# Optimization experiments

Hardware: AMD Instinct MI355X
Metric: run time of the kernel (lower is better)

The kernel has to match this reference:

```python
import jax, jax.numpy as jnp
import numpy as np

N, E, DIN, DH, DE, DOUT, G = 100000, 1600000, 64, 128, 16, 1, 256

def setup_inputs() -> dict:
    key = jax.random.key(0)
    ks = jax.random.split(key, 16)
    p = lambda k, s: (jax.random.normal(k, s, dtype=jnp.float32) * 0.05)
    return {
        "x": jax.random.normal(ks[0], (N, DIN), dtype=jnp.float32),
        "edge_index": jax.random.randint(ks[1], (2, E), 0, N, dtype=jnp.int64),
        "edge_attr": jax.random.normal(ks[2], (E, DE), dtype=jnp.float32),
        "batch": jnp.sort(jax.random.randint(ks[3], (N,), 0, G, dtype=jnp.int64)),
        # GINEConv 1: edge lin (edge_dim -> input_dim) + mlp1 (DIN->DH->DH)
        "ew1": p(ks[4], (DIN, DE)), "eb1": p(ks[5], (DIN,)),
        "w1a": p(ks[6], (DH, DIN)), "b1a": p(ks[7], (DH,)),
        "w1b": p(ks[8], (DH, DH)), "b1b": p(ks[9], (DH,)),
        # GINEConv 2: edge lin (edge_dim -> hidden_dim) + mlp2 (DH->DH->DH)
        "ew2": p(ks[10], (DH, DE)), "eb2": p(ks[11], (DH,)),
        "w2a": p(ks[12], (DH, DH)), "b2a": p(ks[13], (DH,)),
        "w2b": p(ks[14], (DH, DH)), "b2b": p(ks[15], (DH,)),
        "wf": p(jax.random.fold_in(key, 99), (DOUT, DH)),
        "bf": jnp.zeros((DOUT,), dtype=jnp.float32),
    }

def _gine(x, src, dst, edge_attr, ew, eb, wa, ba, wb, bb):
    # message = relu(x[src] + Lin(edge_attr)); sum-aggregate at dst; eps=0
    msg = jax.nn.relu(x[src] + edge_attr @ ew.T + eb)          # [E, D]
    aggr = jax.ops.segment_sum(msg, dst, num_segments=x.shape[0])
    h = x + aggr                                               # (1+eps)*x + aggr, eps=0
    h = jax.nn.relu(h @ wa.T + ba)
    return h @ wb.T + bb

def reference(x, edge_index, edge_attr, batch, ew1, eb1, w1a, b1a, w1b, b1b,
              ew2, eb2, w2a, b2a, w2b, b2b, wf, bf):
    src, dst = edge_index[0], edge_index[1]
    h = _gine(x, src, dst, edge_attr, ew1, eb1, w1a, b1a, w1b, b1b)
    h = jax.nn.relu(h)  # dropout is identity in eval mode
    h = _gine(h, src, dst, edge_attr, ew2, eb2, w2a, b2a, w2b, b2b)
    h = jax.nn.relu(h)
    # global mean pool over graphs
    sums = jax.ops.segment_sum(h, batch, num_segments=G)       # [G, DH]
    cnts = jax.ops.segment_sum(jnp.ones((h.shape[0],), h.dtype), batch, num_segments=G)
    pooled = sums / jnp.maximum(cnts, 1.0)[:, None]
    return pooled @ wf.T + bf                                  # [G, DOUT]
```

## Files before the change

kernel.cpp:

```cpp
#include <hip/hip_runtime.h>

#define DINc 64
#define DHc  128
#define DEc  16
#define Gc   256
#define Rrep 64
#define SCB  1024

typedef unsigned short u16;
typedef unsigned int   u32;
typedef __attribute__((ext_vector_type(8))) short bf8;
typedef __attribute__((ext_vector_type(4))) short bf4;
typedef __attribute__((ext_vector_type(4))) float f4;
typedef __attribute__((ext_vector_type(4))) unsigned int u32x4;
typedef _Float16 h2t __attribute__((ext_vector_type(2)));

__device__ __forceinline__ u16 f2b(float f) {
  u32 u = __builtin_bit_cast(u32, f);
  u32 r = u + 0x7FFFu + ((u >> 16) & 1u);
  return (u16)(r >> 16);
}
__device__ __forceinline__ float b2f(u16 h) {
  u32 u = ((u32)h) << 16;
  return __builtin_bit_cast(float, u);
}
__device__ __forceinline__ u32 pkbf(float a, float b) {
  return ((u32)f2b(b) << 16) | (u32)f2b(a);
}
__device__ __forceinline__ u32 pkh(float a, float b) {
  u16 ua = __builtin_bit_cast(u16, (_Float16)a);
  u16 ub = __builtin_bit_cast(u16, (_Float16)b);
  return ((u32)ub << 16) | ua;
}
__device__ __forceinline__ float fd2(u32 a, u32 b, float c) {
  return __builtin_amdgcn_fdot2(__builtin_bit_cast(h2t, a),
                                __builtin_bit_cast(h2t, b), c, false);
}

__global__ __launch_bounds__(256) void k_cvtw(const float* __restrict__ w1a,
                                              const float* __restrict__ w1b,
                                              const float* __restrict__ w2a,
                                              const float* __restrict__ w2b,
                                              u16* __restrict__ dst) {
  const int i = blockIdx.x * 256 + threadIdx.x;
  const float* src; int off;
  if      (i < 1024) { src = w1a; off = i; }
  else if (i < 3072) { src = w1b; off = i - 1024; }
  else if (i < 5120) { src = w2a; off = i - 3072; }
  else if (i < 7168) { src = w2b; off = i - 5120; }
  else return;
  float4 f0 = *(const float4*)(src + (size_t)off * 8);
  float4 f1 = *(const float4*)(src + (size_t)off * 8 + 4);
  bf8 v;
  v[0]=(short)f2b(f0.x); v[1]=(short)f2b(f0.y); v[2]=(short)f2b(f0.z); v[3]=(short)f2b(f0.w);
  v[4]=(short)f2b(f1.x); v[5]=(short)f2b(f1.y); v[6]=(short)f2b(f1.z); v[7]=(short)f2b(f1.w);
  *(bf8*)(dst + (size_t)i * 8) = v;
}

__global__ __launch_bounds__(256) void k_hist(const int* __restrict__ dstA, const int nE,
                                              int* __restrict__ deg) {
  for (int i = blockIdx.x * 256 + threadIdx.x; i < nE; i += gridDim.x * 256)
    atomicAdd(&deg[dstA[i]], 1);
}

__global__ __launch_bounds__(256) void k_scan_blk(const int* __restrict__ deg,
                                                  int* __restrict__ bsum, const int nN) {
  const int b = blockIdx.x, t = threadIdx.x;
  const int i0 = b * SCB + t * 4;
  int s = 0;
  #pragma unroll
  for (int q = 0; q < 4; ++q) { const int i = i0 + q; if (i < nN) s += deg[i]; }
  #pragma unroll
  for (int off = 32; off > 0; off >>= 1) s += __shfl_down(s, off);
  __shared__ int ws[4];
  if ((t & 63) == 0) ws[t >> 6] = s;
  __syncthreads();
  if (t == 0) bsum[b] = ws[0] + ws[1] + ws[2] + ws[3];
}

__global__ __launch_bounds__(256) void k_scan_fin(const int* __restrict__ deg,
                                                  const int* __restrict__ bsum,
                                                  int* __restrict__ rowptr,
                                                  const int nN, const int nB) {
  const int b = blockIdx.x, t = threadIdx.x;
  int p = 0;
  for (int i = t; i < b; i += 256) p += bsum[i];
  #pragma unroll
  for (int off = 32; off > 0; off >>= 1) p += __shfl_down(p, off);
  __shared__ int ws[4];
  __shared__ int sc[256];
  if ((t & 63) == 0) ws[t >> 6] = p;
  const int i0 = b * SCB + t * 4;
  int vals[4]; int s = 0;
  #pragma unroll
  for (int q = 0; q < 4; ++q) { const int i = i0 + q; vals[q] = (i < nN) ? deg[i] : 0; s += vals[q]; }
  sc[t] = s;
  __syncthreads();
  const int boff = ws[0] + ws[1] + ws[2] + ws[3];
  for (int off = 1; off < 256; off <<= 1) {
    int u = (t >= off) ? sc[t - off] : 0;
    __syncthreads();
    sc[t] += u;
    __syncthreads();
  }
  int run = boff + sc[t] - s;
  #pragma unroll
  for (int q = 0; q < 4; ++q) { const int i = i0 + q; if (i < nN) rowptr[i] = run; run += vals[q]; }
  if (b == nB - 1 && t == 255) rowptr[nN] = run;
}

__global__ __launch_bounds__(256) void k_fill(const int* __restrict__ dstA,
                                              const int* __restrict__ srcA, const int nE,
                                              const int* __restrict__ rowptr,
                                              int* __restrict__ cursor, int2* __restrict__ csr,
                                              int* __restrict__ dstC) {
  for (int i = blockIdx.x * 256 + threadIdx.x; i < nE; i += gridDim.x * 256) {
    const int d = dstA[i];
    const int pos = atomicAdd(&cursor[d], 1);
    csr[rowptr[d] + pos] = make_int2(i, srcA[i]);
    dstC[rowptr[d] + pos] = d;
  }
}

__global__ __launch_bounds__(256) void k_bea(const int2* __restrict__ csr,
                                             const float* __restrict__ ea,
                                             u16* __restrict__ ea16, const int nE) {
  for (int i = blockIdx.x * 256 + threadIdx.x; i < nE; i += gridDim.x * 256) {
    const int e = csr[i].x;
    const float4* ep = (const float4*)(ea + (size_t)e * 16);
    float4 a0 = ep[0], a1 = ep[1], a2 = ep[2], a3 = ep[3];
    u32x4 w0, w1;
    w0[0] = pkh(a0.x, a0.y); w0[1] = pkh(a0.z, a0.w);
    w0[2] = pkh(a1.x, a1.y); w0[3] = pkh(a1.z, a1.w);
    w1[0] = pkh(a2.x, a2.y); w1[1] = pkh(a2.z, a2.w);
    w1[2] = pkh(a3.x, a3.y); w1[3] = pkh(a3.z, a3.w);
    *(u32x4*)(ea16 + (size_t)i * 16)     = w0;
    *(u32x4*)(ea16 + (size_t)i * 16 + 8) = w1;
  }
}

__global__ __launch_bounds__(256) void k_cnt_bs(const int* __restrict__ batch,
                                                float* __restrict__ cnts, const int nN) {
  const int g = threadIdx.x;
  if (g >= Gc) return;
  int lo = 0, hi = nN;
  while (lo < hi) { int m = (lo + hi) >> 1; if (batch[m] < g) lo = m + 1; else hi = m; }
  int lo2 = lo, hi2 = nN;
  while (lo2 < hi2) { int m = (lo2 + hi2) >> 1; if (batch[m] < g + 1) lo2 = m + 1; else hi2 = m; }
  cnts[g] = (float)(lo2 - lo);
}

__device__ __forceinline__ int span_lb(const int* __restrict__ rp, int nN, int target) {
  int lo = 0, hi = nN;
  while (lo < hi) { int m = (lo + hi) >> 1; if (rp[m] < target) lo = m + 1; else hi = m; }
  return lo;
}

template<int D, bool XF>
__global__ __launch_bounds__(256) void gather_f16(
    const float* __restrict__ xf, const u16* __restrict__ xb,
    const int2* __restrict__ csr, const int* __restrict__ dstC,
    const u16* __restrict__ ea16,
    const float* __restrict__ ewg, const float* __restrict__ ebg,
    const int* __restrict__ rowptr, u16* __restrict__ agg, const int nN, const int nE)
{
  constexpr int PL = D / 64;
  __shared__ u32 eas[4][64][8];
  const int lane = threadIdx.x & 63, wv = threadIdx.x >> 6;
  u32 (*E)[8] = eas[wv];

  u32 wpk[8 * PL]; float ebr[PL];
  #pragma unroll
  for (int p = 0; p < PL; ++p) {
    const int d = lane * PL + p;
    ebr[p] = ebg[d];
    #pragma unroll
    for (int j = 0; j < 8; ++j)
      wpk[p * 8 + j] = pkh(ewg[d * 16 + 2 * j], ewg[d * 16 + 2 * j + 1]);
  }

  const int wgid = blockIdx.x * 4 + wv;
  const int nw   = gridDim.x * 4;
  const int t0 = (int)((long long)nE * wgid / nw);
  const int t1 = (int)((long long)nE * (wgid + 1) / nw);
  const int n0 = span_lb(rowptr, nN, t0);
  const int n1 = (wgid == nw - 1) ? nN : span_lb(rowptr, nN, t1);
  if (n0 >= n1) return;
  const int e0 = rowptr[n0], e1 = rowptr[n1];

  float acc0 = 0.f, acc1 = 0.f;
  int cur = n0 - 1;

  for (int chunk = e0; chunk < e1; chunk += 64) {
    const int cnt = min(64, e1 - chunk);
    int2 es = (lane < cnt) ? csr[chunk + lane] : make_int2(0, 0);
    int dl  = (lane < cnt) ? dstC[chunk + lane] : -1;
    const int pd = __shfl_up(dl, 1);
    const bool bnd = (lane < cnt) && (dl != ((lane == 0) ? cur : pd));
    const unsigned long long bmask = __ballot(bnd);

    if (lane < cnt) {
      u32x4 a = *(const u32x4*)(ea16 + (size_t)(chunk + lane) * 16);
      u32x4 b = *(const u32x4*)(ea16 + (size_t)(chunk + lane) * 16 + 8);
      *(u32x4*)&E[lane][0] = a;
      *(u32x4*)&E[lane][4] = b;
    }

    for (int i = 0; i < cnt; i += 8) {
      const int g = min(8, cnt - i);
      float xs[8]; u32 xv[8];
      #pragma unroll
      for (int q = 0; q < 8; ++q) {
        if (q < g) {
          const int s = __builtin_amdgcn_readlane(es.y, i + q);
          if (XF) xs[q] = xf[(size_t)s * 64 + lane];
          else    xv[q] = *(const u32*)(xb + (size_t)s * 128 + lane * 2);
        }
      }
      #pragma unroll
      for (int q = 0; q < 8; ++q) {
        if (q < g) {
          const int e = i + q;
          if ((bmask >> e) & 1ull) {
            const int nd = __builtin_amdgcn_readlane(dl, e);
            if (cur >= n0) {
              if (PL == 2) *(u32*)(agg + (size_t)cur * 128 + lane * 2) = pkbf(acc0, acc1);
              else         agg[(size_t)cur * 64 + lane] = f2b(acc0);
            }
            for (int m = cur + 1; m < nd; ++m) {
              if (PL == 2) *(u32*)(agg + (size_t)m * 128 + lane * 2) = 0u;
              else         agg[(size_t)m * 64 + lane] = 0;
            }
            acc0 = 0.f; acc1 = 0.f;
            cur = nd;
          }
          u32x4 r0 = *(const u32x4*)&E[e][0];
          u32x4 r1 = *(const u32x4*)&E[e][4];
          if (PL == 1) {
            float v = ebr[0];
            v = fd2(r0[0], wpk[0], v); v = fd2(r0[1], wpk[1], v);
            v = fd2(r0[2], wpk[2], v); v = fd2(r0[3], wpk[3], v);
            v = fd2(r1[0], wpk[4], v); v = fd2(r1[1], wpk[5], v);
            v = fd2(r1[2], wpk[6], v); v = fd2(r1[3], wpk[7], v);
            const float xval = XF ? xs[q] : b2f((u16)(xv[q] & 0xFFFFu));
            acc0 += fmaxf(xval + v, 0.f);
          } else {
            float v0 = ebr[0], v1 = ebr[1];
            v0 = fd2(r0[0], wpk[0], v0); v1 = fd2(r0[0], wpk[8],  v1);
            v0 = fd2(r0[1], wpk[1], v0); v1 = fd2(r0[1], wpk[9],  v1);
            v0 = fd2(r0[2], wpk[2], v0); v1 = fd2(r0[2], wpk[10], v1);
            v0 = fd2(r0[3], wpk[3], v0); v1 = fd2(r0[3], wpk[11], v1);
            v0 = fd2(r1[0], wpk[4], v0); v1 = fd2(r1[0], wpk[12], v1);
            v0 = fd2(r1[1], wpk[5], v0); v1 = fd2(r1[1], wpk[13], v1);
            v0 = fd2(r1[2], wpk[6], v0); v1 = fd2(r1[2], wpk[14], v1);
            v0 = fd2(r1[3], wpk[7], v0); v1 = fd2(r1[3], wpk[15], v1);
            acc0 += fmaxf(b2f((u16)(xv[q] & 0xFFFFu)) + v0, 0.f);
            acc1 += fmaxf(b2f((u16)(xv[q] >> 16)) + v1, 0.f);
          }
        }
      }
    }
  }
  if (cur >= n0) {
    if (PL == 2) *(u32*)(agg + (size_t)cur * 128 + lane * 2) = pkbf(acc0, acc1);
    else         agg[(size_t)cur * 64 + lane] = f2b(acc0);
  }
  for (int m = cur + 1; m < n1; ++m) {
    if (PL == 2) *(u32*)(agg + (size_t)m * 128 + lane * 2) = 0u;
    else         agg[(size_t)m * 64 + lane] = 0;
  }
}

template<int IN, bool XF>
__global__ __launch_bounds__(256) void k_l1(
    const float* __restrict__ xf, const u16* __restrict__ xbm,
    const u16* __restrict__ agb,
    const u16* __restrict__ waB, const float* __restrict__ ba,
    u16* __restrict__ tout, const int nN)
{
  __shared__ u16 wa_s[DHc * IN];
  __shared__ float ba_s[DHc];
  const int tid = threadIdx.x;
  constexpr int INC = IN / 8;
  for (int c = tid; c < DHc * INC; c += 256) {
    const int row = c / INC, kc = (c % INC) * 8;
    bf8 v = *(const bf8*)(waB + (size_t)row * IN + kc);
    *(bf8*)(wa_s + ((row * IN + kc) ^ ((row & 7) << 3))) = v;
  }
  if (tid < DHc) ba_s[tid] = ba[tid];
  __syncthreads();
  const int lane = tid & 63, wv = tid >> 6;
  const int lr = lane & 15, l4 = lane >> 4;
  const int nT = (nN + 15) >> 4;
  for (int tile = blockIdx.x * 4 + wv; tile < nT; tile += gridDim.x * 4) {
    const int node = tile * 16 + lr;
    const int n = min(node, nN - 1);
    bf8 bfr[IN / 32];
    #pragma unroll
    for (int ks = 0; ks < IN / 32; ++ks) {
      const int k0 = ks * 32 + l4 * 8;
      bf8 av = *(const bf8*)(agb + (size_t)n * IN + k0);
      bf8 v;
      if (XF) {
        float4 x0 = *(const float4*)(xf + (size_t)n * IN + k0);
        float4 x1 = *(const float4*)(xf + (size_t)n * IN + k0 + 4);
        v[0] = (short)f2b(x0.x + b2f((u16)av[0]));
        v[1] = (short)f2b(x0.y + b2f((u16)av[1]));
        v[2] = (short)f2b(x0.z + b2f((u16)av[2]));
        v[3] = (short)f2b(x0.w + b2f((u16)av[3]));
        v[4] = (short)f2b(x1.x + b2f((u16)av[4]));
        v[5] = (short)f2b(x1.y + b2f((u16)av[5]));
        v[6] = (short)f2b(x1.z + b2f((u16)av[6]));
        v[7] = (short)f2b(x1.w + b2f((u16)av[7]));
      } else {
        bf8 xv = *(const bf8*)(xbm + (size_t)n * IN + k0);
        #pragma unroll
        for (int j = 0; j < 8; ++j)
          v[j] = (short)f2b(b2f((u16)xv[j]) + b2f((u16)av[j]));
      }
      bfr[ks] = v;
    }
    const bool valid = node < nN;
    #pragma unroll
    for (int jt = 0; jt < 8; ++jt) {
      f4 c = {0.f, 0.f, 0.f, 0.f};
      #pragma unroll
      for (int ks = 0; ks < IN / 32; ++ks) {
        bf8 a = *(const bf8*)(wa_s + (((jt * 16 + lr) * IN + ks * 32 + l4 * 8) ^ ((lr & 7) << 3)));
        c = __builtin_amdgcn_mfma_f32_16x16x32_bf16(a, bfr[ks], c, 0, 0, 0);
      }
      if (valid) {
        float4 bav = *(const float4*)(ba_s + jt * 16 + l4 * 4);
        bf4 tv;
        tv[0] = (short)f2b(fmaxf(c[0] + bav.x, 0.f));
        tv[1] = (short)f2b(fmaxf(c[1] + bav.y, 0.f));
        tv[2] = (short)f2b(fmaxf(c[2] + bav.z, 0.f));
        tv[3] = (short)f2b(fmaxf(c[3] + bav.w, 0.f));
        *(bf4*)(tout + (size_t)node * DHc + jt * 16 + l4 * 4) = tv;
      }
    }
  }
}

template<bool FINAL>
__global__ __launch_bounds__(256) void k_l2(
    const u16* __restrict__ tin, const u16* __restrict__ wbB,
    const float* __restrict__ bb, u16* __restrict__ hout,
    const int* __restrict__ batch, float* __restrict__ sums, const int nN)
{
  __shared__ u16 wb_s[DHc * DHc];
  __shared__ float bb_s[DHc];
  const int tid = threadIdx.x;
  for (int c = tid; c < DHc * 16; c += 256) {
    const int row = c >> 4, kc = (c & 15) * 8;
    bf8 v = *(const bf8*)(wbB + (size_t)row * DHc + kc);
    *(bf8*)(wb_s + ((row * DHc + kc) ^ ((row & 7) << 3))) = v;
  }
  if (tid < DHc) bb_s[tid] = bb[tid];
  __syncthreads();
  const int lane = tid & 63, wv = tid >> 6;
  const int lr = lane & 15, l4 = lane >> 4;
  const int nT = (nN + 15) >> 4;
  const int gw0 = blockIdx.x * 4 + wv;
  const int rep = gw0 & (Rrep - 1);
  for (int tile = gw0; tile < nT; tile += gridDim.x * 4) {
    const int node0 = tile * 16;
    const int node = node0 + lr;
    const int n = min(node, nN - 1);
    bf8 tb[4];
    #pragma unroll
    for (int ks = 0; ks < 4; ++ks)
      tb[ks] = *(const bf8*)(tin + (size_t)n * DHc + ks * 32 + l4 * 8);
    const bool valid = node < nN;
    int gl = 0, g0 = 0; bool uni = false;
    if (FINAL) {
      gl = batch[n];
      g0 = __shfl(gl, 0);
      uni = __all(gl == g0) && (node0 + 16 <= nN);
    }
    #pragma unroll
    for (int jt = 0; jt < 8; ++jt) {
      f4 c = {0.f, 0.f, 0.f, 0.f};
      #pragma unroll
      for (int ks = 0; ks < 4; ++ks) {
        bf8 a = *(const bf8*)(wb_s + (((jt * 16 + lr) * DHc + ks * 32 + l4 * 8) ^ ((lr & 7) << 3)));
        c = __builtin_amdgcn_mfma_f32_16x16x32_bf16(a, tb[ks], c, 0, 0, 0);
      }
      float4 bbv = *(const float4*)(bb_s + jt * 16 + l4 * 4);
      float o0 = fmaxf(c[0] + bbv.x, 0.f);
      float o1 = fmaxf(c[1] + bbv.y, 0.f);
      float o2 = fmaxf(c[2] + bbv.z, 0.f);
      float o3 = fmaxf(c[3] + bbv.w, 0.f);
      if (!FINAL) {
        if (valid) {
          bf4 hv;
          hv[0] = (short)f2b(o0); hv[1] = (short)f2b(o1);
          hv[2] = (short)f2b(o2); hv[3] = (short)f2b(o3);
          *(bf4*)(hout + (size_t)node * DHc + jt * 16 + l4 * 4) = hv;
        }
      } else {
        if (uni) {
          #pragma unroll
          for (int off = 1; off < 16; off <<= 1) {
            o0 += __shfl_xor(o0, off);
            o1 += __shfl_xor(o1, off);
            o2 += __shfl_xor(o2, off);
            o3 += __shfl_xor(o3, off);
          }
          if (lr == 0) {
            float* dp = sums + ((size_t)rep * Gc + g0) * DHc + jt * 16 + l4 * 4;
            atomicAdd(dp + 0, o0); atomicAdd(dp + 1, o1);
            atomicAdd(dp + 2, o2); atomicAdd(dp + 3, o3);
          }
        } else if (valid) {
          float* dp = sums + ((size_t)rep * Gc + gl) * DHc + jt * 16 + l4 * 4;
          atomicAdd(dp + 0, o0); atomicAdd(dp + 1, o1);
          atomicAdd(dp + 2, o2); atomicAdd(dp + 3, o3);
        }
      }
    }
  }
}

__global__ __launch_bounds__(128) void pool_final(
    const float* __restrict__ sums, const float* __restrict__ cnts,
    const float* __restrict__ wf, const float* __restrict__ bf,
    float* __restrict__ out)
{
  const int g = blockIdx.x;
  const int j = threadIdx.x;
  float s = 0.f;
  for (int r = 0; r < Rrep; ++r) s += sums[((size_t)r * Gc + g) * DHc + j];
  const float ct = fmaxf(cnts[g], 1.f);
  __shared__ float red[128];
  red[j] = (s / ct) * wf[j];
  __syncthreads();
  for (int off = 64; off > 0; off >>= 1) { if (j < off) red[j] += red[j + off]; __syncthreads(); }
  if (j == 0) out[g] = red[0] + bf[0];
}

extern "C" void kernel_launch(void* const* d_in, const int* in_sizes, int n_in,
                              void* d_out, int out_size, void* d_ws, size_t ws_size,
                              hipStream_t stream) {
  const float* x    = (const float*)d_in[0];
  const int*   ei   = (const int*)d_in[1];
  const float* ea   = (const float*)d_in[2];
  const int*   batch= (const int*)d_in[3];
  const float* ew1  = (const float*)d_in[4];
  const float* eb1  = (const float*)d_in[5];
  const float* w1a  = (const float*)d_in[6];
  const float* b1a  = (const float*)d_in[7];
  const float* w1b  = (const float*)d_in[8];
  const float* b1b  = (const float*)d_in[9];
  const float* ew2  = (const float*)d_in[10];
  const float* eb2  = (const float*)d_in[11];
  const float* w2a  = (const float*)d_in[12];
  const float* b2a  = (const float*)d_in[13];
  const float* w2b  = (const float*)d_in[14];
  const float* b2b  = (const float*)d_in[15];
  const float* wf   = (const float*)d_in[16];
  const float* bf   = (const float*)d_in[17];
  float* out = (float*)d_out;

  const int nN = in_sizes[0] / DINc;
  const int nE = in_sizes[1] / 2;
  const int* srcA = ei;
  const int* dstA = ei + nE;

  char* wsb = (char*)d_ws;
  size_t o = 0;
  u16*   h1b    = (u16*)  (wsb + o); o += (size_t)nN * DHc * 2;
  u16*   tbuf   = (u16*)  (wsb + o); o += (size_t)nN * DHc * 2;
  u16*   agb    = (u16*)  (wsb + o); o += (size_t)nN * DHc * 2;
  float* sums   = (float*)(wsb + o); o += (size_t)Rrep * Gc * DHc * 4;
  float* cnts   = (float*)(wsb + o); o += (size_t)Gc * 4;
  int*   deg    = (int*)  (wsb + o); o += (size_t)nN * 4;
  int*   cursor = (int*)  (wsb + o); o += (size_t)nN * 4;
  int*   rowptr = (int*)  (wsb + o); o += (size_t)(nN + 1) * 4;
  int*   bsum   = (int*)  (wsb + o); o += (size_t)((nN + SCB - 1) / SCB) * 4; o = (o + 15) & ~(size_t)15;
  int2*  csr    = (int2*) (wsb + o); o += (size_t)nE * 8;
  int*   dstC   = (int*)  (wsb + o); o += (size_t)nE * 4; o = (o + 15) & ~(size_t)15;
  u16*   ea16   = (u16*)  (wsb + o); o += (size_t)nE * 16 * 2;
  u16*   wts    = (u16*)  (wsb + o); o += (size_t)57344 * 2;
  u16* w1ab = wts;
  u16* w1bb = wts + 8192;
  u16* w2ab = wts + 8192 + 16384;
  u16* w2bb = wts + 8192 + 32768;
  (void)ws_size; (void)n_in; (void)out_size;

  hipMemsetAsync(sums, 0, (size_t)Rrep * Gc * DHc * 4 + (size_t)Gc * 4, stream);
  hipMemsetAsync(deg, 0, (size_t)nN * 8, stream);

  const int nB = (nN + SCB - 1) / SCB;
  k_cvtw<<<28, 256, 0, stream>>>(w1a, w1b, w2a, w2b, wts);
  k_hist<<<1024, 256, 0, stream>>>(dstA, nE, deg);
  k_scan_blk<<<nB, 256, 0, stream>>>(deg, bsum, nN);
  k_scan_fin<<<nB, 256, 0, stream>>>(deg, bsum, rowptr, nN, nB);
  k_fill<<<1024, 256, 0, stream>>>(dstA, srcA, nE, rowptr, cursor, csr, dstC);
  k_bea<<<2048, 256, 0, stream>>>(csr, ea, ea16, nE);
  k_cnt_bs<<<1, 256, 0, stream>>>(batch, cnts, nN);

  const int nT = (nN + 15) / 16;
  const int mg = (nT + 3) / 4;
  gather_f16<DINc, true><<<2048, 256, 0, stream>>>(x, nullptr, csr, dstC, ea16,
                                                   ew1, eb1, rowptr, agb, nN, nE);
  k_l1<DINc, true><<<mg, 256, 0, stream>>>(x, nullptr, agb, w1ab, b1a, tbuf, nN);
  k_l2<false><<<mg, 256, 0, stream>>>(tbuf, w1bb, b1b, h1b, nullptr, nullptr, nN);
  gather_f16<DHc, false><<<2048, 256, 0, stream>>>(nullptr, h1b, csr, dstC, ea16,
                                                   ew2, eb2, rowptr, agb, nN, nE);
  k_l1<DHc, false><<<mg, 256, 0, stream>>>(nullptr, h1b, agb, w2ab, b2a, tbuf, nN);
  k_l2<true><<<mg, 256, 0, stream>>>(tbuf, w2bb, b2b, nullptr, batch, sums, nN);
  pool_final<<<Gc, 128, 0, stream>>>(sums, cnts, wf, bf, out);
}
```

Baseline: 599.4 us.

## Fuse edge-attr conversion into CSR fill and iterate gather by rowptr

The CSR fill kernel now also converts edge attributes to fp16 and writes them at the sorted position, which removes the separate k_bea pass and the int2 csr/dstC arrays. The gather kernel walks destination nodes via rowptr instead of detecting segment boundaries from a per-edge dst array, so it reads less index data per edge. The graph-count kernel is folded into pool_final. The trade-off is scattered 32-byte writes in the fill kernel and more per-node control flow in the gather.

Measured after the change: 642.5 us. 1.07x slower.

```diff
diff --git a/kernel.cpp b/kernel.cpp
--- a/kernel.cpp
+++ b/kernel.cpp
@@ -23,6 +23,12 @@
 __device__ __forceinline__ float b2f(u16 h) {
   u32 u = ((u32)h) << 16;
   return __builtin_bit_cast(float, u);
+}
+__device__ __forceinline__ float blo(u32 v) {
+  return __builtin_bit_cast(float, v << 16);
+}
+__device__ __forceinline__ float bhi(u32 v) {
+  return __builtin_bit_cast(float, v & 0xFFFF0000u);
 }
 __device__ __forceinline__ u32 pkbf(float a, float b) {
   return ((u32)f2b(b) << 16) | (u32)f2b(a);
@@ -110,44 +116,26 @@
 }
 
 __global__ __launch_bounds__(256) void k_fill(const int* __restrict__ dstA,
-                                              const int* __restrict__ srcA, const int nE,
+                                              const int* __restrict__ srcA,
+                                              const float* __restrict__ ea, const int nE,
                                               const int* __restrict__ rowptr,
-                                              int* __restrict__ cursor, int2* __restrict__ csr,
-                                              int* __restrict__ dstC) {
+                                              int* __restrict__ cursor,
+                                              int* __restrict__ srcC,
+                                              u16* __restrict__ ea16) {
   for (int i = blockIdx.x * 256 + threadIdx.x; i < nE; i += gridDim.x * 256) {
     const int d = dstA[i];
-    const int pos = atomicAdd(&cursor[d], 1);
-    csr[rowptr[d] + pos] = make_int2(i, srcA[i]);
-    dstC[rowptr[d] + pos] = d;
-  }
-}
-
-__global__ __launch_bounds__(256) void k_bea(const int2* __restrict__ csr,
-                                             const float* __restrict__ ea,
-                                             u16* __restrict__ ea16, const int nE) {
-  for (int i = blockIdx.x * 256 + threadIdx.x; i < nE; i += gridDim.x * 256) {
-    const int e = csr[i].x;
-    const float4* ep = (const float4*)(ea + (size_t)e * 16);
+    const int pos = rowptr[d] + atomicAdd(&cursor[d], 1);
+    srcC[pos] = srcA[i];
+    const float4* ep = (const float4*)(ea + (size_t)i * 16);
     float4 a0 = ep[0], a1 = ep[1], a2 = ep[2], a3 = ep[3];
     u32x4 w0, w1;
     w0[0] = pkh(a0.x, a0.y); w0[1] = pkh(a0.z, a0.w);
     w0[2] = pkh(a1.x, a1.y); w0[3] = pkh(a1.z, a1.w);
     w1[0] = pkh(a2.x, a2.y); w1[1] = pkh(a2.z, a2.w);
     w1[2] = pkh(a3.x, a3.y); w1[3] = pkh(a3.z, a3.w);
-    *(u32x4*)(ea16 + (size_t)i * 16)     = w0;
-    *(u32x4*)(ea16 + (size_t)i * 16 + 8) = w1;
-  }
-}
-
-__global__ __launch_bounds__(256) void k_cnt_bs(const int* __restrict__ batch,
-                                                float* __restrict__ cnts, const int nN) {
-  const int g = threadIdx.x;
-  if (g >= Gc) return;
-  int lo = 0, hi = nN;
-  while (lo < hi) { int m = (lo + hi) >> 1; if (batch[m] < g) lo = m + 1; else hi = m; }
-  int lo2 = lo, hi2 = nN;
-  while (lo2 < hi2) { int m = (lo2 + hi2) >> 1; if (batch[m] < g + 1) lo2 = m + 1; else hi2 = m; }
-  cnts[g] = (float)(lo2 - lo);
+    *(u32x4*)(ea16 + (size_t)pos * 16)     = w0;
+    *(u32x4*)(ea16 + (size_t)pos * 16 + 8) = w1;
+  }
 }
 
 __device__ __forceinline__ int span_lb(const int* __restrict__ rp, int nN, int target) {
@@ -157,12 +145,12 @@
 }
 
 template<int D, bool XF>
-__global__ __launch_bounds__(256) void gather_f16(
+__global__ __launch_bounds__(256) void gather3(
     const float* __restrict__ xf, const u16* __restrict__ xb,
-    const int2* __restrict__ csr, const int* __restrict__ dstC,
-    const u16* __restrict__ ea16,
+    const int* __restrict__ srcC, const u16* __restrict__ ea16,
     const float* __restrict__ ewg, const float* __restrict__ ebg,
-    const int* __restrict__ rowptr, u16* __restrict__ agg, const int nN, const int nE)
+    const int* __restrict__ rowptr, u16* __restrict__ agg,
+    const int nN, const int nE)
 {
   constexpr int PL = D / 64;
   __shared__ u32 eas[4][64][8];
@@ -186,88 +174,81 @@
   const int n0 = span_lb(rowptr, nN, t0);
   const int n1 = (wgid == nw - 1) ? nN : span_lb(rowptr, nN, t1);
   if (n0 >= n1) return;
-  const int e0 = rowptr[n0], e1 = rowptr[n1];
-
-  float acc0 = 0.f, acc1 = 0.f;
-  int cur = n0 - 1;
-
-  for (int chunk = e0; chunk < e1; chunk += 64) {
-    const int cnt = min(64, e1 - chunk);
-    int2 es = (lane < cnt) ? csr[chunk + lane] : make_int2(0, 0);
-    int dl  = (lane < cnt) ? dstC[chunk + lane] : -1;
-    const int pd = __shfl_up(dl, 1);
-    const bool bnd = (lane < cnt) && (dl != ((lane == 0) ? cur : pd));
-    const unsigned long long bmask = __ballot(bnd);
-
-    if (lane < cnt) {
-      u32x4 a = *(const u32x4*)(ea16 + (size_t)(chunk + lane) * 16);
-      u32x4 b = *(const u32x4*)(ea16 + (size_t)(chunk + lane) * 16 + 8);
-      *(u32x4*)&E[lane][0] = a;
-      *(u32x4*)&E[lane][4] = b;
-    }
-
-    for (int i = 0; i < cnt; i += 8) {
-      const int g = min(8, cnt - i);
-      float xs[8]; u32 xv[8];
-      #pragma unroll
-      for (int q = 0; q < 8; ++q) {
-        if (q < g) {
-          const int s = __builtin_amdgcn_readlane(es.y, i + q);
-          if (XF) xs[q] = xf[(size_t)s * 64 + lane];
-          else    xv[q] = *(const u32*)(xb + (size_t)s * 128 + lane * 2);
+  const int e1 = rowptr[n1];
+
+  int nwb = n0;
+  int rpv = rowptr[min(nwb + lane, n1)];
+  int wbase = 0, wend = -1;
+  int sidl = 0;
+
+  for (int n = n0; n < n1; ++n) {
+    int rel = n - nwb;
+    if (rel >= 63) {
+      nwb = n;
+      rpv = rowptr[min(nwb + lane, n1)];
+      rel = 0;
+    }
+    int p         = __builtin_amdgcn_readlane(rpv, rel);
+    const int end = __builtin_amdgcn_readlane(rpv, rel + 1);
+    float acc0 = 0.f, acc1 = 0.f;
+    while (p < end) {
+      if (p >= wend) {
+        const int cw = min(64, e1 - p);
+        if (lane < cw) {
+          sidl = srcC[p + lane];
+          u32x4 a = *(const u32x4*)(ea16 + (size_t)(p + lane) * 16);
+          u32x4 b = *(const u32x4*)(ea16 + (size_t)(p + lane) * 16 + 8);
+          *(u32x4*)&E[lane][0] = a;
+          *(u32x4*)&E[lane][4] = b;
         }
-      }
-      #pragma unroll
-      for (int q = 0; q < 8; ++q) {
-        if (q < g) {
-          const int e = i + q;
-          if ((bmask >> e) & 1ull) {
-            const int nd = __builtin_amdgcn_readlane(dl, e);
-            if (cur >= n0) {
-              if (PL == 2) *(u32*)(agg + (size_t)cur * 128 + lane * 2) = pkbf(acc0, acc1);
-              else         agg[(size_t)cur * 64 + lane] = f2b(acc0);
-            }
-            for (int m = cur + 1; m < nd; ++m) {
-              if (PL == 2) *(u32*)(agg + (size_t)m * 128 + lane * 2) = 0u;
-              else         agg[(size_t)m * 64 + lane] = 0;
-            }
-            acc0 = 0.f; acc1 = 0.f;
-            cur = nd;
-          }
-          u32x4 r0 = *(const u32x4*)&E[e][0];
-          u32x4 r1 = *(const u32x4*)&E[e][4];
-          if (PL == 1) {
-            float v = ebr[0];
-            v = fd2(r0[0], wpk[0], v); v = fd2(r0[1], wpk[1], v);
-            v = fd2(r0[2], wpk[2], v); v = fd2(r0[3], wpk[3], v);
-            v = fd2(r1[0], wpk[4], v); v = fd2(r1[1], wpk[5], v);
-            v = fd2(r1[2], wpk[6], v); v = fd2(r1[3], wpk[7], v);
-            const float xval = XF ? xs[q] : b2f((u16)(xv[q] & 0xFFFFu));
-            acc0 += fmaxf(xval + v, 0.f);
-          } else {
-            float v0 = ebr[0], v1 = ebr[1];
-            v0 = fd2(r0[0], wpk[0], v0); v1 = fd2(r0[0], wpk[8],  v1);
-            v0 = fd2(r0[1], wpk[1], v0); v1 = fd2(r0[1], wpk[9],  v1);
-            v0 = fd2(r0[2], wpk[2], v0); v1 = fd2(r0[2], wpk[10], v1);
-            v0 = fd2(r0[3], wpk[3], v0); v1 = fd2(r0[3], wpk[11], v1);
-            v0 = fd2(r1[0], wpk[4], v0); v1 = fd2(r1[0], wpk[12], v1);
-            v0 = fd2(r1[1], wpk[5], v0); v1 = fd2(r1[1], wpk[13], v1);
-            v0 = fd2(r1[2], wpk[6], v0); v1 = fd2(r1[2], wpk[14], v1);
-            v0 = fd2(r1[3], wpk[7], v0); v1 = fd2(r1[3], wpk[15], v1);
-            acc0 += fmaxf(b2f((u16)(xv[q] & 0xFFFFu)) + v0, 0.f);
-            acc1 += fmaxf(b2f((u16)(xv[q] >> 16)) + v1, 0.f);
+        wbase = p; wend = p + cw;
+      }
+      const int k = min(end, wend) - p;
+      for (int i = 0; i < k; i += 8) {
+        const int g = min(8, k - i);
+        u32 xv[8]; float xs[8];
+        #pragma unroll
+        for (int q = 0; q < 8; ++q) {
+          if (q < g) {
+            const int s = __builtin_amdgcn_readlane(sidl, p - wbase + i + q);
+            if (XF) xs[q] = xf[(size_t)s * D + lane];
+            else    xv[q] = *(const u32*)(xb + (size_t)s * D + lane * 2);
           }
         }
-      }
-    }
-  }
-  if (cur >= n0) {
-    if (PL == 2) *(u32*)(agg + (size_t)cur * 128 + lane * 2) = pkbf(acc0, acc1);
-    else         agg[(size_t)cur * 64 + lane] = f2b(acc0);
-  }
-  for (int m = cur + 1; m < n1; ++m) {
-    if (PL == 2) *(u32*)(agg + (size_t)m * 128 + lane * 2) = 0u;
-    else         agg[(size_t)m * 64 + lane] = 0;
+        #pragma unroll
+        for (int q = 0; q < 8; ++q) {
+          if (q < g) {
+            const int e = p - wbase + i + q;
+            u32x4 r0 = *(const u32x4*)&E[e][0];
+            u32x4 r1 = *(const u32x4*)&E[e][4];
+            if (PL == 1) {
+              float v = ebr[0];
+              v = fd2(r0[0], wpk[0], v); v = fd2(r0[1], wpk[1], v);
+              v = fd2(r0[2], wpk[2], v); v = fd2(r0[3], wpk[3], v);
+              v = fd2(r1[0], wpk[4], v); v = fd2(r1[1], wpk[5], v);
+              v = fd2(r1[2], wpk[6], v); v = fd2(r1[3], wpk[7], v);
+              const float xval = XF ? xs[q] : blo(xv[q]);
+              acc0 += fmaxf(xval + v, 0.f);
+            } else {
+              float v0 = ebr[0], v1 = ebr[1];
+              v0 = fd2(r0[0], wpk[0], v0); v1 = fd2(r0[0], wpk[8],  v1);
+              v0 = fd2(r0[1], wpk[1], v0); v1 = fd2(r0[1], wpk[9],  v1);
+              v0 = fd2(r0[2], wpk[2], v0); v1 = fd2(r0[2], wpk[10], v1);
+              v0 = fd2(r0[3], wpk[3], v0); v1 = fd2(r0[3], wpk[11], v1);
+              v0 = fd2(r1[0], wpk[4], v0); v1 = fd2(r1[0], wpk[12], v1);
+              v0 = fd2(r1[1], wpk[5], v0); v1 = fd2(r1[1], wpk[13], v1);
+              v0 = fd2(r1[2], wpk[6], v0); v1 = fd2(r1[2], wpk[14], v1);
+              v0 = fd2(r1[3], wpk[7], v0); v1 = fd2(r1[3], wpk[15], v1);
+              acc0 += fmaxf(blo(xv[q]) + v0, 0.f);
+              acc1 += fmaxf(bhi(xv[q]) + v1, 0.f);
+            }
+          }
+        }
+      }
+      p += k;
+    }
+    if (PL == 2) *(u32*)(agg + (size_t)n * 128 + lane * 2) = pkbf(acc0, acc1);
+    else         agg[(size_t)n * 64 + lane] = f2b(acc0);
   }
 }
 
@@ -423,15 +404,19 @@
 }
 
 __global__ __launch_bounds__(128) void pool_final(
-    const float* __restrict__ sums, const float* __restrict__ cnts,
+    const float* __restrict__ sums, const int* __restrict__ batch,
     const float* __restrict__ wf, const float* __restrict__ bf,
-    float* __restrict__ out)
+    float* __restrict__ out, const int nN)
 {
   const int g = blockIdx.x;
   const int j = threadIdx.x;
   float s = 0.f;
   for (int r = 0; r < Rrep; ++r) s += sums[((size_t)r * Gc + g) * DHc + j];
-  const float ct = fmaxf(cnts[g], 1.f);
+  int lo = 0, hi = nN;
+  while (lo < hi) { int m = (lo + hi) >> 1; if (batch[m] < g) lo = m + 1; else hi = m; }
+  int lo2 = lo, hi2 = nN;
+  while (lo2 < hi2) { int m = (lo2 + hi2) >> 1; if (batch[m] < g + 1) lo2 = m + 1; else hi2 = m; }
+  const float ct = fmaxf((float)(lo2 - lo), 1.f);
   __shared__ float red[128];
   red[j] = (s / ct) * wf[j];
   __syncthreads();
@@ -473,13 +458,11 @@
   u16*   tbuf   = (u16*)  (wsb + o); o += (size_t)nN * DHc * 2;
   u16*   agb    = (u16*)  (wsb + o); o += (size_t)nN * DHc * 2;
   float* sums   = (float*)(wsb + o); o += (size_t)Rrep * Gc * DHc * 4;
-  float* cnts   = (float*)(wsb + o); o += (size_t)Gc * 4;
   int*   deg    = (int*)  (wsb + o); o += (size_t)nN * 4;
   int*   cursor = (int*)  (wsb + o); o += (size_t)nN * 4;
   int*   rowptr = (int*)  (wsb + o); o += (size_t)(nN + 1) * 4;
   int*   bsum   = (int*)  (wsb + o); o += (size_t)((nN + SCB - 1) / SCB) * 4; o = (o + 15) & ~(size_t)15;
-  int2*  csr    = (int2*) (wsb + o); o += (size_t)nE * 8;
-  int*   dstC   = (int*)  (wsb + o); o += (size_t)nE * 4; o = (o + 15) & ~(size_t)15;
+  int*   srcC   = (int*)  (wsb + o); o += (size_t)nE * 4; o = (o + 15) & ~(size_t)15;
   u16*   ea16   = (u16*)  (wsb + o); o += (size_t)nE * 16 * 2;
   u16*   wts    = (u16*)  (wsb + o); o += (size_t)57344 * 2;
   u16* w1ab = wts;
@@ -488,7 +471,7 @@
   u16* w2bb = wts + 8192 + 32768;
   (void)ws_size; (void)n_in; (void)out_size;
 
-  hipMemsetAsync(sums, 0, (size_t)Rrep * Gc * DHc * 4 + (size_t)Gc * 4, stream);
+  hipMemsetAsync(sums, 0, (size_t)Rrep * Gc * DHc * 4, stream);
   hipMemsetAsync(deg, 0, (size_t)nN * 8, stream);
 
   const int nB = (nN + SCB - 1) / SCB;
@@ -496,19 +479,17 @@
   k_hist<<<1024, 256, 0, stream>>>(dstA, nE, deg);
   k_scan_blk<<<nB, 256, 0, stream>>>(deg, bsum, nN);
   k_scan_fin<<<nB, 256, 0, stream>>>(deg, bsum, rowptr, nN, nB);
-  k_fill<<<1024, 256, 0, stream>>>(dstA, srcA, nE, rowptr, cursor, csr, dstC);
-  k_bea<<<2048, 256, 0, stream>>>(csr, ea, ea16, nE);
-  k_cnt_bs<<<1, 256, 0, stream>>>(batch, cnts, nN);
+  k_fill<<<1024, 256, 0, stream>>>(dstA, srcA, ea, nE, rowptr, cursor, srcC, ea16);
 
   const int nT = (nN + 15) / 16;
   const int mg = (nT + 3) / 4;
-  gather_f16<DINc, true><<<2048, 256, 0, stream>>>(x, nullptr, csr, dstC, ea16,
-                                                   ew1, eb1, rowptr, agb, nN, nE);
+  gather3<DINc, true><<<2048, 256, 0, stream>>>(x, nullptr, srcC, ea16,
+                                                ew1, eb1, rowptr, agb, nN, nE);
   k_l1<DINc, true><<<mg, 256, 0, stream>>>(x, nullptr, agb, w1ab, b1a, tbuf, nN);
   k_l2<false><<<mg, 256, 0, stream>>>(tbuf, w1bb, b1b, h1b, nullptr, nullptr, nN);
-  gather_f16<DHc, false><<<2048, 256, 0, stream>>>(nullptr, h1b, csr, dstC, ea16,
-                                                   ew2, eb2, rowptr, agb, nN, nE);
+  gather3<DHc, false><<<2048, 256, 0, stream>>>(nullptr, h1b, srcC, ea16,
+                                                ew2, eb2, rowptr, agb, nN, nE);
   k_l1<DHc, false><<<mg, 256, 0, stream>>>(nullptr, h1b, agb, w2ab, b2a, tbuf, nN);
   k_l2<true><<<mg, 256, 0, stream>>>(tbuf, w2bb, b2b, nullptr, batch, sums, nN);
-  pool_final<<<Gc, 128, 0, stream>>>(sums, cnts, wf, bf, out);
-}
+  pool_final<<<Gc, 128, 0, stream>>>(sums, batch, wf, bf, out, nN);
+}
```
